# Performance work log

Measured on AMD Instinct MI355X. Metric: run time of the kernel, lower is better.

The kernel has to match this reference:

```python
import jax, jax.numpy as jnp
import numpy as np

E = 256
H_HEADS = 8
HD = E // H_HEADS
NEG = -1e9


def setup_inputs() -> dict:
    key = jax.random.key(0)
    ks = jax.random.split(key, 16)
    B, Q, Hh, Ww = 16, 100, 64, 64
    S = Hh * Ww
    std = 1.0 / np.sqrt(E)
    inp = {
        "query_features": jax.random.normal(ks[0], (B, Q, E), jnp.float32),
        "image_features": jax.random.normal(ks[1], (B, E, Hh, Ww), jnp.float32),
        "mask": jax.random.randint(ks[2], (B, Q, Hh, Ww), 0, 2) > 0,
        "pos_query_embeddings": jax.random.normal(ks[3], (B, Q, E), jnp.float32),
        "pos_image_embeddings": jax.random.normal(ks[4], (B, S, E), jnp.float32),
        "Wq": jax.random.normal(ks[5], (E, E), jnp.float32) * std,
        "bq": jnp.zeros((E,), jnp.float32),
        "Wk": jax.random.normal(ks[6], (E, E), jnp.float32) * std,
        "bk": jnp.zeros((E,), jnp.float32),
        "Wv": jax.random.normal(ks[7], (E, E), jnp.float32) * std,
        "bv": jnp.zeros((E,), jnp.float32),
        "Wo": jax.random.normal(ks[8], (E, E), jnp.float32) * std,
        "bo": jnp.zeros((E,), jnp.float32),
    }
    return inp


def reference(query_features, image_features, mask, pos_query_embeddings,
              pos_image_embeddings, Wq, bq, Wk, bk, Wv, bv, Wo, bo):
    B, _, Hh, Ww = image_features.shape
    Q = query_features.shape[1]
    S = Hh * Ww
    # (B, S, E)
    img = jnp.transpose(image_features.reshape(B, E, S), (0, 2, 1))
    q = (query_features + pos_query_embeddings) @ Wq.T + bq  # (B,Q,E)
    k = (img + pos_image_embeddings) @ Wk.T + bk              # (B,S,E)
    v = img @ Wv.T + bv                                       # (B,S,E)
    q = q.reshape(B, Q, H_HEADS, HD).transpose(0, 2, 1, 3)    # (B,H,Q,D)
    k = k.reshape(B, S, H_HEADS, HD).transpose(0, 2, 1, 3)    # (B,H,S,D)
    v = v.reshape(B, S, H_HEADS, HD).transpose(0, 2, 1, 3)
    scale = 1.0 / jnp.sqrt(jnp.asarray(HD, q.dtype))
    scores = jnp.einsum('bhqd,bhsd->bhqs', q, k) * scale
    amask = mask.reshape(B, 1, Q, S)
    scores = jnp.where(amask, scores, NEG)
    attn = jax.nn.softmax(scores, axis=-1)
    out = jnp.einsum('bhqs,bhsd->bhqd', attn, v)
    out = out.transpose(0, 2, 1, 3).reshape(B, Q, E)
    return out @ Wo.T + bo
```

## Files before the change

kernel.cpp:

```cpp
#include <hip/hip_runtime.h>
#include <math.h>

#define BB 16
#define QQ 100
#define EE 256
#define NH 8
#define HD 32
#define SS 4096
#define QP 128
#define NZ 8
#define SCHUNK (SS / NZ)
#define M0 8.0f

typedef _Float16 half8_t __attribute__((ext_vector_type(8)));
typedef _Float16 half4_t __attribute__((ext_vector_type(4)));
typedef float floatx4 __attribute__((ext_vector_type(4)));

__global__ __launch_bounds__(256) void prep_kernel(
    const float* __restrict__ qf,  const float* __restrict__ pq,
    const float* __restrict__ Wq,  const float* __restrict__ bq,
    _Float16* __restrict__ q16,
    const float* __restrict__ Wk,  const float* __restrict__ Wv,
    _Float16* __restrict__ wk16a,  _Float16* __restrict__ wv16a,
    const int* __restrict__ mask,  unsigned* __restrict__ mbits)
{
    const int bid = blockIdx.x;
    const int t = threadIdx.x;

    if (bid < 200) {
        const float scale = 0.17677669529663687f;
        const int row0 = bid * 8;
        __shared__ float xs[8][256];
        #pragma unroll
        for (int p = 0; p < 8; ++p) {
            int idx = t + p * 256;
            int f = idx & 255, j = idx >> 8;
            size_t g = (size_t)(row0 + j) * EE + f;
            xs[j][f] = qf[g] + pq[g];
        }
        __syncthreads();
        const int e = t;
        const float* wrow = Wq + (size_t)e * EE;
        float acc[8];
        const float bv = bq[e];
        #pragma unroll
        for (int j = 0; j < 8; ++j) acc[j] = bv;
        #pragma unroll 4
        for (int f4 = 0; f4 < 64; ++f4) {
            float4 w4 = *(const float4*)(wrow + f4 * 4);
            #pragma unroll
            for (int j = 0; j < 8; ++j) {
                float4 x4 = *(const float4*)&xs[j][f4 * 4];
                acc[j] = fmaf(w4.x, x4.x, acc[j]);
                acc[j] = fmaf(w4.y, x4.y, acc[j]);
                acc[j] = fmaf(w4.z, x4.z, acc[j]);
                acc[j] = fmaf(w4.w, x4.w, acc[j]);
            }
        }
        #pragma unroll
        for (int j = 0; j < 8; ++j)
            q16[(size_t)(row0 + j) * EE + e] = (_Float16)(acc[j] * scale);
    } else if (bid < 264) {
        int gid = (bid - 200) * 256 + t;
        int m = gid & 8191;
        const float* src = (gid < 8192) ? Wk : Wv;
        _Float16* dst = (gid < 8192) ? wk16a : wv16a;
        int li = m & 15, gg = (m >> 4) & 3, jj = (m >> 6) & 1;
        int kk = (m >> 7) & 7, w = (m >> 10) & 7;
        int e = w * 32 + jj * 16 + li;
        int f0 = kk * 32 + gg * 8;
        float4 a0 = *(const float4*)&src[(size_t)e * EE + f0];
        float4 a1 = *(const float4*)&src[(size_t)e * EE + f0 + 4];
        half8_t h;
        h[0]=(_Float16)a0.x; h[1]=(_Float16)a0.y; h[2]=(_Float16)a0.z; h[3]=(_Float16)a0.w;
        h[4]=(_Float16)a1.x; h[5]=(_Float16)a1.y; h[6]=(_Float16)a1.z; h[7]=(_Float16)a1.w;
        *(half8_t*)&dst[(size_t)m * 8] = h;
    } else {
        int gid  = (bid - 264) * 256 + t;
        int lane = gid & 63;
        int F    = gid & ~63;
        int s    = (F & (SS - 1)) + lane;
        int qp   = (F >> 12) & (QP - 1);
        int b    = F >> 19;
        int qc   = min(qp, QQ - 1);
        int v    = mask[((size_t)(b * QQ + qc)) * SS + s];
        unsigned long long bal = __ballot(v != 0);
        int w = (F & (SS - 1)) >> 5;
        if (lane == 0)
            mbits[((size_t)(b * (SS / 32) + w)) * QP + qp] = (unsigned)bal;
        if (lane == 32)
            mbits[((size_t)(b * (SS / 32) + w + 1)) * QP + qp] = (unsigned)(bal >> 32);
    }
}

#define KV_STEP(KK, PC, PN, AKC, AVC)                                        \
  {                                                                          \
    float pv0 = PC[l * 33 + w4 + 0];                                         \
    float pv1 = PC[l * 33 + w4 + 1];                                         \
    float pv2 = PC[l * 33 + w4 + 2];                                         \
    float pv3 = PC[l * 33 + w4 + 3];                                         \
    half4_t hk, hv;                                                          \
    hv[0] = (_Float16)iv0; hk[0] = (_Float16)(iv0 + pv0);                    \
    hv[1] = (_Float16)iv1; hk[1] = (_Float16)(iv1 + pv1);                    \
    hv[2] = (_Float16)iv2; hk[2] = (_Float16)(iv2 + pv2);                    \
    hv[3] = (_Float16)iv3; hk[3] = (_Float16)(iv3 + pv3);                    \
    *(half4_t*)&AVC[l * 40 + w4] = hv;                                       \
    *(half4_t*)&AKC[l * 40 + w4] = hk;                                       \
    if ((KK) < 7) {                                                          \
      PN[pr * 33 + pc4 + 0] = pg.x;                                          \
      PN[pr * 33 + pc4 + 1] = pg.y;                                          \
      PN[pr * 33 + pc4 + 2] = pg.z;                                          \
      PN[pr * 33 + pc4 + 3] = pg.w;                                          \
    }                                                                        \
    __syncthreads();                                                         \
    if ((KK) < 6) pg = *(const float4*)(posb + ((KK) + 2) * 32);             \
    if ((KK) < 7) {                                                          \
      iv0 = imgb[(size_t)(((KK) + 1) * 32 + w4 + 0) * SS];                   \
      iv1 = imgb[(size_t)(((KK) + 1) * 32 + w4 + 1) * SS];                   \
      iv2 = imgb[(size_t)(((KK) + 1) * 32 + w4 + 2) * SS];                   \
      iv3 = imgb[(size_t)(((KK) + 1) * 32 + w4 + 3) * SS];                   \
    }                                                                        \
    half8_t wk0 = *(const half8_t*)(wkb + (KK) * 1024);                      \
    half8_t wk1 = *(const half8_t*)(wkb + (KK) * 1024 + 512);                \
    half8_t wv0 = *(const half8_t*)(wvb + (KK) * 1024);                      \
    half8_t wv1 = *(const half8_t*)(wvb + (KK) * 1024 + 512);                \
    half8_t afk0 = *(const half8_t*)&AKC[(0 * 16 + li) * 40 + gg * 8];       \
    half8_t afk1 = *(const half8_t*)&AKC[(1 * 16 + li) * 40 + gg * 8];       \
    half8_t afk2 = *(const half8_t*)&AKC[(2 * 16 + li) * 40 + gg * 8];       \
    half8_t afk3 = *(const half8_t*)&AKC[(3 * 16 + li) * 40 + gg * 8];       \
    acck[0][0] = __builtin_amdgcn_mfma_f32_16x16x32_f16(afk0, wk0, acck[0][0], 0, 0, 0); \
    acck[0][1] = __builtin_amdgcn_mfma_f32_16x16x32_f16(afk0, wk1, acck[0][1], 0, 0, 0); \
    acck[1][0] = __builtin_amdgcn_mfma_f32_16x16x32_f16(afk1, wk0, acck[1][0], 0, 0, 0); \
    acck[1][1] = __builtin_amdgcn_mfma_f32_16x16x32_f16(afk1, wk1, acck[1][1], 0, 0, 0); \
    acck[2][0] = __builtin_amdgcn_mfma_f32_16x16x32_f16(afk2, wk0, acck[2][0], 0, 0, 0); \
    acck[2][1] = __builtin_amdgcn_mfma_f32_16x16x32_f16(afk2, wk1, acck[2][1], 0, 0, 0); \
    acck[3][0] = __builtin_amdgcn_mfma_f32_16x16x32_f16(afk3, wk0, acck[3][0], 0, 0, 0); \
    acck[3][1] = __builtin_amdgcn_mfma_f32_16x16x32_f16(afk3, wk1, acck[3][1], 0, 0, 0); \
    half8_t afv0 = *(const half8_t*)&AVC[(0 * 16 + li) * 40 + gg * 8];       \
    half8_t afv1 = *(const half8_t*)&AVC[(1 * 16 + li) * 40 + gg * 8];       \
    half8_t afv2 = *(const half8_t*)&AVC[(2 * 16 + li) * 40 + gg * 8];       \
    half8_t afv3 = *(const half8_t*)&AVC[(3 * 16 + li) * 40 + gg * 8];       \
    accv[0][0] = __builtin_amdgcn_mfma_f32_16x16x32_f16(afv0, wv0, accv[0][0], 0, 0, 0); \
    accv[0][1] = __builtin_amdgcn_mfma_f32_16x16x32_f16(afv0, wv1, accv[0][1], 0, 0, 0); \
    accv[1][0] = __builtin_amdgcn_mfma_f32_16x16x32_f16(afv1, wv0, accv[1][0], 0, 0, 0); \
    accv[1][1] = __builtin_amdgcn_mfma_f32_16x16x32_f16(afv1, wv1, accv[1][1], 0, 0, 0); \
    accv[2][0] = __builtin_amdgcn_mfma_f32_16x16x32_f16(afv2, wv0, accv[2][0], 0, 0, 0); \
    accv[2][1] = __builtin_amdgcn_mfma_f32_16x16x32_f16(afv2, wv1, accv[2][1], 0, 0, 0); \
    accv[3][0] = __builtin_amdgcn_mfma_f32_16x16x32_f16(afv3, wv0, accv[3][0], 0, 0, 0); \
    accv[3][1] = __builtin_amdgcn_mfma_f32_16x16x32_f16(afv3, wv1, accv[3][1], 0, 0, 0); \
  }

__global__ __launch_bounds__(512, 2) void fused_kv_kernel(
    const float* __restrict__ img,
    const float* __restrict__ pos,
    const _Float16* __restrict__ wk16a, const float* __restrict__ bk,
    const _Float16* __restrict__ wv16a, const float* __restrict__ bv,
    _Float16* __restrict__ kht,
    _Float16* __restrict__ vt)
{
    __shared__ __align__(16) char smem_raw[37376];
    float* posT0 = (float*)smem_raw;
    float* posT1 = posT0 + 64 * 33;
    _Float16* A0k = (_Float16*)(posT1 + 64 * 33);
    _Float16* A0v = A0k + 2560;
    _Float16* A1k = A0v + 2560;
    _Float16* A1v = A1k + 2560;

    const int t  = threadIdx.x;
    const int w  = t >> 6, l = t & 63;
    const int gg = l >> 4, li = l & 15;
    const int pr = t >> 3, pc = t & 7;
    const int w4 = w * 4, pc4 = pc * 4;

    const int m0 = blockIdx.x * 64;
    const int b  = m0 >> 12;
    const int s0 = m0 & (SS - 1);

    const float* imgb = img + (size_t)b * EE * SS + s0 + l;
    const float* posb = pos + ((size_t)(b * SS + s0 + pr)) * EE + pc4;
    const _Float16* wkb = wk16a + ((size_t)(w * 16) * 64 + l) * 8;
    const _Float16* wvb = wv16a + ((size_t)(w * 16) * 64 + l) * 8;

    floatx4 acck[4][2] = {};
    floatx4 accv[4][2] = {};

    float4 pg = *(const float4*)posb;
    float iv0 = imgb[(size_t)(w4 + 0) * SS];
    float iv1 = imgb[(size_t)(w4 + 1) * SS];
    float iv2 = imgb[(size_t)(w4 + 2) * SS];
    float iv3 = imgb[(size_t)(w4 + 3) * SS];
    posT0[pr * 33 + pc4 + 0] = pg.x;
    posT0[pr * 33 + pc4 + 1] = pg.y;
    posT0[pr * 33 + pc4 + 2] = pg.z;
    posT0[pr * 33 + pc4 + 3] = pg.w;
    pg = *(const float4*)(posb + 32);
    __syncthreads();

    #pragma unroll 1
    for (int kp = 0; kp < 4; ++kp) {
        const int kk = kp * 2;
        KV_STEP(kk,     posT0, posT1, A0k, A0v)
        KV_STEP(kk + 1, posT1, posT0, A1k, A1v)
    }

    {
        const size_t khbase = ((size_t)(b * NH + w) * SS + s0) * HD;
        #pragma unroll
        for (int jj = 0; jj < 2; ++jj) {
            int e = w * 32 + jj * 16 + li;
            int d = jj * 16 + li;
            float bj = bk[e];
            #pragma unroll
            for (int i = 0; i < 4; ++i) {
                int s_loc = i * 16 + gg * 4;
                #pragma unroll
                for (int r = 0; r < 4; ++r)
                    kht[khbase + (size_t)(s_loc + r) * HD + d] =
                        (_Float16)(acck[i][jj][r] + bj);
            }
        }
    }

    __syncthreads();
    _Float16* vstage = (_Float16*)smem_raw;
    #pragma unroll
    for (int jj = 0; jj < 2; ++jj) {
        int e_loc = w * 32 + jj * 16 + li;
        float bj = bv[e_loc];
        #pragma unroll
        for (int i = 0; i < 4; ++i) {
            int s_loc = i * 16 + gg * 4;
            half4_t h4;
            #pragma unroll
            for (int r = 0; r < 4; ++r)
                h4[r] = (_Float16)(accv[i][jj][r] + bj);
            *(half4_t*)&vstage[e_loc * 72 + s_loc] = h4;
        }
    }
    __syncthreads();
    #pragma unroll
    for (int c = 0; c < 4; ++c) {
        int row = c * 64 + (t >> 3);
        int so  = (t & 7) * 8;
        half8_t v8 = *(const half8_t*)&vstage[row * 72 + so];
        int hh = row >> 5, dd = row & 31;
        *(half8_t*)(vt + ((((size_t)(b * NH + hh) * (SS / 64) + (s0 >> 6)) * HD + dd) << 6)
                    + so) = v8;
    }
}

__global__ __launch_bounds__(256) void attn_mfma_kernel(
    const _Float16* __restrict__ q16,
    const _Float16* __restrict__ kht,
    const _Float16* __restrict__ vt,
    const unsigned* __restrict__ mbits,
    float* __restrict__ part,
    float* __restrict__ pl)
{
    const int z = blockIdx.x, h = blockIdx.y, b = blockIdx.z;
    const int t = threadIdx.x;
    const int w = t >> 6, l = t & 63;
    const int g = l >> 4, li = l & 15;

    __shared__ _Float16 ks[64 * 40];
    __shared__ _Float16 vs[32 * 72];
    __shared__ _Float16 ps[128 * 72];
    __shared__ unsigned mw[2][QP];

    half8_t qf[2];
    {
        int q0r = min(32 * w + li, QQ - 1);
        int q1r = min(32 * w + 16 + li, QQ - 1);
        qf[0] = *(const half8_t*)(q16 + ((size_t)(b * QQ + q0r)) * EE + h * HD + g * 8);
        qf[1] = *(const half8_t*)(q16 + ((size_t)(b * QQ + q1r)) * EE + h * HD + g * 8);
    }

    float lsum[2][4] = {{0.f}};
    floatx4 accO[2][2] = {};

    for (int it = 0; it < SCHUNK / 64; ++it) {
        const int sblk = z * SCHUNK + it * 64;

        {
            int sl = t >> 2, koff = (t & 3) * 8;
            *(half8_t*)&ks[sl * 40 + koff] =
                *(const half8_t*)(kht + ((size_t)(b * NH + h) * SS + sblk + sl) * HD + koff);
            int dl = t >> 3, soff = (t & 7) * 8;
            *(half8_t*)&vs[dl * 72 + soff] =
                *(const half8_t*)(vt + ((((size_t)(b * NH + h) * (SS / 64) + (sblk >> 6))
                                         * HD + dl) << 6) + soff);
            mw[t >> 7][t & 127] =
                mbits[((size_t)(b * (SS / 32) + (sblk >> 5) + (t >> 7))) * QP + (t & 127)];
        }
        __syncthreads();

        half8_t kf[4];
        #pragma unroll
        for (int st = 0; st < 4; ++st)
            kf[st] = *(const half8_t*)&ks[(st * 16 + li) * 40 + g * 8];
        floatx4 sc[2][4];
        #pragma unroll
        for (int qt = 0; qt < 2; ++qt)
            #pragma unroll
            for (int st = 0; st < 4; ++st) {
                floatx4 zero = {0.f, 0.f, 0.f, 0.f};
                sc[qt][st] = __builtin_amdgcn_mfma_f32_16x16x32_f16(
                    qf[qt], kf[st], zero, 0, 0, 0);
            }

        #pragma unroll
        for (int qt = 0; qt < 2; ++qt) {
            int qrow0 = 32 * w + qt * 16 + 4 * g;
            unsigned w0r[4], w1r[4];
            #pragma unroll
            for (int r = 0; r < 4; ++r) {
                w0r[r] = mw[0][qrow0 + r];
                w1r[r] = mw[1][qrow0 + r];
            }
            #pragma unroll
            for (int st = 0; st < 4; ++st)
                #pragma unroll
                for (int r = 0; r < 4; ++r) {
                    unsigned word = (st < 2) ? w0r[r] : w1r[r];
                    int keep = (word >> ((st & 1) * 16 + li)) & 1;
                    float pv = keep ? __expf(sc[qt][st][r] - M0) : 0.f;
                    _Float16 ph = (_Float16)pv;
                    lsum[qt][r] += (float)ph;
                    ps[(qrow0 + r) * 72 + st * 16 + li] = ph;
                }
        }

        half8_t vb[2][2];
        #pragma unroll
        for (int dt = 0; dt < 2; ++dt) {
            vb[dt][0] = *(const half8_t*)&vs[(dt * 16 + li) * 72 + g * 8];
            vb[dt][1] = *(const half8_t*)&vs[(dt * 16 + li) * 72 + 32 + g * 8];
        }
        #pragma unroll
        for (int qt = 0; qt < 2; ++qt) {
            half8_t a0 = *(const half8_t*)&ps[(32 * w + qt * 16 + li) * 72 + g * 8];
            half8_t a1 = *(const half8_t*)&ps[(32 * w + qt * 16 + li) * 72 + 32 + g * 8];
            #pragma unroll
            for (int dt = 0; dt < 2; ++dt) {
                accO[qt][dt] = __builtin_amdgcn_mfma_f32_16x16x32_f16(
                    a0, vb[dt][0], accO[qt][dt], 0, 0, 0);
                accO[qt][dt] = __builtin_amdgcn_mfma_f32_16x16x32_f16(
                    a1, vb[dt][1], accO[qt][dt], 0, 0, 0);
            }
        }
        __syncthreads();
    }

    #pragma unroll
    for (int qt = 0; qt < 2; ++qt)
        #pragma unroll
        for (int r = 0; r < 4; ++r) {
            float v = lsum[qt][r];
            v += __shfl_xor(v, 1, 64);
            v += __shfl_xor(v, 2, 64);
            v += __shfl_xor(v, 4, 64);
            v += __shfl_xor(v, 8, 64);
            lsum[qt][r] = v;
        }

    const size_t pbase = (((size_t)z * BB + b) * NH + h) * QP;
    #pragma unroll
    for (int qt = 0; qt < 2; ++qt) {
        int qrow0 = 32 * w + qt * 16 + 4 * g;
        #pragma unroll
        for (int r = 0; r < 4; ++r) {
            int qp = qrow0 + r;
            #pragma unroll
            for (int dt = 0; dt < 2; ++dt)
                part[(pbase + qp) * HD + dt * 16 + li] = accO[qt][dt][r];
            if (li == 0) pl[pbase + qp] = lsum[qt][r];
        }
    }
}

__global__ __launch_bounds__(256) void combineproj_kernel(
    const float* __restrict__ part, const float* __restrict__ pl,
    const float* __restrict__ Wo,   const float* __restrict__ bo,
    float* __restrict__ out)
{
    const int row0 = blockIdx.x * 8;
    const int t = threadIdx.x;
    __shared__ float xs[8][256];

    const int h = t >> 5, d = t & 31;
    #pragma unroll
    for (int j = 0; j < 8; ++j) {
        int row = row0 + j;
        int b = row / QQ, qp = row % QQ;
        float L = 0.f, O = 0.f;
        #pragma unroll
        for (int z = 0; z < NZ; ++z) {
            size_t idx = (((size_t)z * BB + b) * NH + h) * QP + qp;
            L += pl[idx];
            O += part[idx * HD + d];
        }
        xs[j][t] = O / fmaxf(L, 1e-30f);
    }
    __syncthreads();

    const int e = t;
    const float* wrow = Wo + (size_t)e * EE;
    float acc[8];
    const float bv = bo[e];
    #pragma unroll
    for (int j = 0; j < 8; ++j) acc[j] = bv;

    #pragma unroll 4
    for (int f4 = 0; f4 < 64; ++f4) {
        float4 w4 = *(const float4*)(wrow + f4 * 4);
        #pragma unroll
        for (int j = 0; j < 8; ++j) {
            float4 x4 = *(const float4*)&xs[j][f4 * 4];
            acc[j] = fmaf(w4.x, x4.x, acc[j]);
            acc[j] = fmaf(w4.y, x4.y, acc[j]);
            acc[j] = fmaf(w4.z, x4.z, acc[j]);
            acc[j] = fmaf(w4.w, x4.w, acc[j]);
        }
    }
    #pragma unroll
    for (int j = 0; j < 8; ++j)
        out[(size_t)(row0 + j) * EE + e] = acc[j];
}

extern "C" void kernel_launch(void* const* d_in, const int* in_sizes, int n_in,
                              void* d_out, int out_size, void* d_ws, size_t ws_size,
                              hipStream_t stream)
{
    const float* qf   = (const float*)d_in[0];
    const float* img  = (const float*)d_in[1];
    const int*   mask = (const int*)  d_in[2];
    const float* pq   = (const float*)d_in[3];
    const float* pimg = (const float*)d_in[4];
    const float* Wq   = (const float*)d_in[5];
    const float* bq   = (const float*)d_in[6];
    const float* Wk   = (const float*)d_in[7];
    const float* bk   = (const float*)d_in[8];
    const float* Wv   = (const float*)d_in[9];
    const float* bv   = (const float*)d_in[10];
    const float* Wo   = (const float*)d_in[11];
    const float* bo   = (const float*)d_in[12];
    float* out = (float*)d_out;

    const size_t MSE = (size_t)BB * SS * EE;

    _Float16* kht  = (_Float16*)d_ws;
    _Float16* vtb  = kht + MSE;
    _Float16* q16  = vtb + MSE;
    unsigned* mbits = (unsigned*)(q16 + (size_t)BB * QQ * EE);
    float* part = (float*)(mbits + (size_t)BB * (SS / 32) * QP);
    float* pl   = part + (size_t)NZ * BB * NH * QP * HD;
    _Float16* wk16a = (_Float16*)(pl + (size_t)NZ * BB * NH * QP);
    _Float16* wv16a = wk16a + (size_t)EE * EE;

    prep_kernel<<<264 + (BB * QP * SS) / 256, 256, 0, stream>>>(
        qf, pq, Wq, bq, q16, Wk, Wv, wk16a, wv16a, mask, mbits);
    fused_kv_kernel<<<BB * SS / 64, 512, 0, stream>>>(
        img, pimg, wk16a, bk, wv16a, bv, kht, vtb);
    attn_mfma_kernel<<<dim3(NZ, NH, BB), 256, 0, stream>>>(
        q16, kht, vtb, mbits, part, pl);
    combineproj_kernel<<<BB * QQ / 8, 256, 0, stream>>>(part, pl, Wo, bo, out);
}
```

Measured before the change: 281.4 us.

## Split attention by query tiles with per-wave private S streams, drop split-S partials

Restructures the attention kernel so each block handles a 32-query tile for one (b,h), with two wave pairs each walking alternate 64-key blocks over the full sequence. Each wave loads its own K/V slice into private LDS, so the per-iteration block barriers are gone. Mask words are read straight from global memory instead of being staged in LDS. The two S-halves are reduced in shared memory and the normalized output is written directly, so the combine kernel only loads rows before the output projection. This removes the NZ-way split-S partial buffers and their reduction, at the cost of reloading K/V for each of the 4 query tiles and having less per-wave reuse.

```diff
diff --git a/kernel.cpp b/kernel.cpp
--- a/kernel.cpp
+++ b/kernel.cpp
@@ -8,8 +8,6 @@
 #define HD 32
 #define SS 4096
 #define QP 128
-#define NZ 8
-#define SCHUNK (SS / NZ)
 #define M0 8.0f
 
 typedef _Float16 half8_t __attribute__((ext_vector_type(8)));
@@ -249,157 +247,148 @@
     }
 }
 
-__global__ __launch_bounds__(256) void attn_mfma_kernel(
+__global__ __launch_bounds__(256) void attn_kernel(
     const _Float16* __restrict__ q16,
     const _Float16* __restrict__ kht,
     const _Float16* __restrict__ vt,
     const unsigned* __restrict__ mbits,
-    float* __restrict__ part,
-    float* __restrict__ pl)
+    float* __restrict__ abuf)
 {
-    const int z = blockIdx.x, h = blockIdx.y, b = blockIdx.z;
+    const int qq = blockIdx.x, h = blockIdx.y, b = blockIdx.z;
     const int t = threadIdx.x;
     const int w = t >> 6, l = t & 63;
     const int g = l >> 4, li = l & 15;
-
-    __shared__ _Float16 ks[64 * 40];
-    __shared__ _Float16 vs[32 * 72];
-    __shared__ _Float16 ps[128 * 72];
-    __shared__ unsigned mw[2][QP];
-
-    half8_t qf[2];
+    const int wq = w >> 1, ws = w & 1;
+
+    __shared__ _Float16 smem[4 * 6016];
+    _Float16* Ks = smem + w * 6016;
+    _Float16* Vs = Ks + 2560;
+    _Float16* Ps = Vs + 2304;
+
+    const int qrowbase = qq * 32 + wq * 16;
+
+    half8_t qf;
     {
-        int q0r = min(32 * w + li, QQ - 1);
-        int q1r = min(32 * w + 16 + li, QQ - 1);
-        qf[0] = *(const half8_t*)(q16 + ((size_t)(b * QQ + q0r)) * EE + h * HD + g * 8);
-        qf[1] = *(const half8_t*)(q16 + ((size_t)(b * QQ + q1r)) * EE + h * HD + g * 8);
-    }
-
-    float lsum[2][4] = {{0.f}};
-    floatx4 accO[2][2] = {};
-
-    for (int it = 0; it < SCHUNK / 64; ++it) {
-        const int sblk = z * SCHUNK + it * 64;
-
+        int qr = min(qrowbase + li, QQ - 1);
+        qf = *(const half8_t*)(q16 + ((size_t)(b * QQ + qr)) * EE + h * HD + g * 8);
+    }
+
+    const _Float16* kbase = kht + (size_t)(b * NH + h) * SS * HD;
+    const _Float16* vbase = vt + (size_t)(b * NH + h) * (SS / 64) * (HD * 64);
+    const unsigned* mbase = mbits + (size_t)b * (SS / 32) * QP + qrowbase + 4 * g;
+
+    float lsum[4] = {0.f, 0.f, 0.f, 0.f};
+    floatx4 accO[2] = {};
+
+    #pragma unroll 1
+    for (int it = ws; it < 64; it += 2) {
+        const int sblk = it * 64;
         {
-            int sl = t >> 2, koff = (t & 3) * 8;
-            *(half8_t*)&ks[sl * 40 + koff] =
-                *(const half8_t*)(kht + ((size_t)(b * NH + h) * SS + sblk + sl) * HD + koff);
-            int dl = t >> 3, soff = (t & 7) * 8;
-            *(half8_t*)&vs[dl * 72 + soff] =
-                *(const half8_t*)(vt + ((((size_t)(b * NH + h) * (SS / 64) + (sblk >> 6))
-                                         * HD + dl) << 6) + soff);
-            mw[t >> 7][t & 127] =
-                mbits[((size_t)(b * (SS / 32) + (sblk >> 5) + (t >> 7))) * QP + (t & 127)];
-        }
-        __syncthreads();
-
-        half8_t kf[4];
+            const _Float16* src = kbase + (size_t)sblk * HD + l * HD;
+            #pragma unroll
+            for (int q4 = 0; q4 < 4; ++q4)
+                *(half8_t*)&Ks[l * 40 + q4 * 8] = *(const half8_t*)(src + q4 * 8);
+        }
+        {
+            int dl = l >> 1, so = (l & 1) * 32;
+            const _Float16* src = vbase + (size_t)it * (HD * 64) + dl * 64 + so;
+            #pragma unroll
+            for (int q4 = 0; q4 < 4; ++q4)
+                *(half8_t*)&Vs[dl * 72 + so + q4 * 8] = *(const half8_t*)(src + q4 * 8);
+        }
+        uint4 mw0 = *(const uint4*)(mbase + (size_t)(it * 2) * QP);
+        uint4 mw1 = *(const uint4*)(mbase + (size_t)(it * 2 + 1) * QP);
+
+        half8_t kf0 = *(const half8_t*)&Ks[(0 * 16 + li) * 40 + g * 8];
+        half8_t kf1 = *(const half8_t*)&Ks[(1 * 16 + li) * 40 + g * 8];
+        half8_t kf2 = *(const half8_t*)&Ks[(2 * 16 + li) * 40 + g * 8];
+        half8_t kf3 = *(const half8_t*)&Ks[(3 * 16 + li) * 40 + g * 8];
+        floatx4 zero = {0.f, 0.f, 0.f, 0.f};
+        floatx4 sc[4];
+        sc[0] = __builtin_amdgcn_mfma_f32_16x16x32_f16(qf, kf0, zero, 0, 0, 0);
+        sc[1] = __builtin_amdgcn_mfma_f32_16x16x32_f16(qf, kf1, zero, 0, 0, 0);
+        sc[2] = __builtin_amdgcn_mfma_f32_16x16x32_f16(qf, kf2, zero, 0, 0, 0);
+        sc[3] = __builtin_amdgcn_mfma_f32_16x16x32_f16(qf, kf3, zero, 0, 0, 0);
+
+        unsigned mr0[4] = {mw0.x, mw0.y, mw0.z, mw0.w};
+        unsigned mr1[4] = {mw1.x, mw1.y, mw1.z, mw1.w};
         #pragma unroll
         for (int st = 0; st < 4; ++st)
-            kf[st] = *(const half8_t*)&ks[(st * 16 + li) * 40 + g * 8];
-        floatx4 sc[2][4];
-        #pragma unroll
-        for (int qt = 0; qt < 2; ++qt)
-            #pragma unroll
-            for (int st = 0; st < 4; ++st) {
-                floatx4 zero = {0.f, 0.f, 0.f, 0.f};
-                sc[qt][st] = __builtin_amdgcn_mfma_f32_16x16x32_f16(
-                    qf[qt], kf[st], zero, 0, 0, 0);
+            #pragma unroll
+            for (int r = 0; r < 4; ++r) {
+                unsigned word = (st < 2) ? mr0[r] : mr1[r];
+                int keep = (word >> ((st & 1) * 16 + li)) & 1;
+                float pv = keep ? __expf(sc[st][r] - M0) : 0.f;
+                _Float16 ph = (_Float16)pv;
+                lsum[r] += (float)ph;
+                Ps[(4 * g + r) * 72 + st * 16 + li] = ph;
             }
 
-        #pragma unroll
-        for (int qt = 0; qt < 2; ++qt) {
-            int qrow0 = 32 * w + qt * 16 + 4 * g;
-            unsigned w0r[4], w1r[4];
-            #pragma unroll
-            for (int r = 0; r < 4; ++r) {
-                w0r[r] = mw[0][qrow0 + r];
-                w1r[r] = mw[1][qrow0 + r];
+        half8_t a0 = *(const half8_t*)&Ps[li * 72 + g * 8];
+        half8_t a1 = *(const half8_t*)&Ps[li * 72 + 32 + g * 8];
+        #pragma unroll
+        for (int dt = 0; dt < 2; ++dt) {
+            half8_t vb0 = *(const half8_t*)&Vs[(dt * 16 + li) * 72 + g * 8];
+            half8_t vb1 = *(const half8_t*)&Vs[(dt * 16 + li) * 72 + 32 + g * 8];
+            accO[dt] = __builtin_amdgcn_mfma_f32_16x16x32_f16(a0, vb0, accO[dt], 0, 0, 0);
+            accO[dt] = __builtin_amdgcn_mfma_f32_16x16x32_f16(a1, vb1, accO[dt], 0, 0, 0);
+        }
+    }
+
+    #pragma unroll
+    for (int r = 0; r < 4; ++r) {
+        float v = lsum[r];
+        v += __shfl_xor(v, 1, 64);
+        v += __shfl_xor(v, 2, 64);
+        v += __shfl_xor(v, 4, 64);
+        v += __shfl_xor(v, 8, 64);
+        lsum[r] = v;
+    }
+
+    __syncthreads();
+    float* redO = (float*)smem;
+    float* redl = redO + 2 * 16 * 32;
+    if (ws == 1) {
+        #pragma unroll
+        for (int r = 0; r < 4; ++r) {
+            int q = 4 * g + r;
+            redO[(wq * 16 + q) * 32 + li]      = accO[0][r];
+            redO[(wq * 16 + q) * 32 + 16 + li] = accO[1][r];
+            if (li == 0) redl[wq * 16 + q] = lsum[r];
+        }
+    }
+    __syncthreads();
+    if (ws == 0) {
+        #pragma unroll
+        for (int r = 0; r < 4; ++r) {
+            int q = 4 * g + r;
+            int qglob = qrowbase + q;
+            float L = lsum[r] + redl[wq * 16 + q];
+            float invL = 1.f / fmaxf(L, 1e-30f);
+            if (qglob < QQ) {
+                float o0 = (accO[0][r] + redO[(wq * 16 + q) * 32 + li]) * invL;
+                float o1 = (accO[1][r] + redO[(wq * 16 + q) * 32 + 16 + li]) * invL;
+                abuf[((size_t)(b * QQ + qglob)) * EE + h * HD + li]      = o0;
+                abuf[((size_t)(b * QQ + qglob)) * EE + h * HD + 16 + li] = o1;
             }
-            #pragma unroll
-            for (int st = 0; st < 4; ++st)
-                #pragma unroll
-                for (int r = 0; r < 4; ++r) {
-                    unsigned word = (st < 2) ? w0r[r] : w1r[r];
-                    int keep = (word >> ((st & 1) * 16 + li)) & 1;
-                    float pv = keep ? __expf(sc[qt][st][r] - M0) : 0.f;
-                    _Float16 ph = (_Float16)pv;
-                    lsum[qt][r] += (float)ph;
-                    ps[(qrow0 + r) * 72 + st * 16 + li] = ph;
-                }
-        }
-
-        half8_t vb[2][2];
-        #pragma unroll
-        for (int dt = 0; dt < 2; ++dt) {
-            vb[dt][0] = *(const half8_t*)&vs[(dt * 16 + li) * 72 + g * 8];
-            vb[dt][1] = *(const half8_t*)&vs[(dt * 16 + li) * 72 + 32 + g * 8];
-        }
-        #pragma unroll
-        for (int qt = 0; qt < 2; ++qt) {
-            half8_t a0 = *(const half8_t*)&ps[(32 * w + qt * 16 + li) * 72 + g * 8];
-            half8_t a1 = *(const half8_t*)&ps[(32 * w + qt * 16 + li) * 72 + 32 + g * 8];
-            #pragma unroll
-            for (int dt = 0; dt < 2; ++dt) {
-                accO[qt][dt] = __builtin_amdgcn_mfma_f32_16x16x32_f16(
-                    a0, vb[dt][0], accO[qt][dt], 0, 0, 0);
-                accO[qt][dt] = __builtin_amdgcn_mfma_f32_16x16x32_f16(
-                    a1, vb[dt][1], accO[qt][dt], 0, 0, 0);
-            }
-        }
-        __syncthreads();
-    }
-
-    #pragma unroll
-    for (int qt = 0; qt < 2; ++qt)
-        #pragma unroll
-        for (int r = 0; r < 4; ++r) {
-            float v = lsum[qt][r];
-            v += __shfl_xor(v, 1, 64);
-            v += __shfl_xor(v, 2, 64);
-            v += __shfl_xor(v, 4, 64);
-            v += __shfl_xor(v, 8, 64);
-            lsum[qt][r] = v;
-        }
-
-    const size_t pbase = (((size_t)z * BB + b) * NH + h) * QP;
-    #pragma unroll
-    for (int qt = 0; qt < 2; ++qt) {
-        int qrow0 = 32 * w + qt * 16 + 4 * g;
-        #pragma unroll
-        for (int r = 0; r < 4; ++r) {
-            int qp = qrow0 + r;
-            #pragma unroll
-            for (int dt = 0; dt < 2; ++dt)
-                part[(pbase + qp) * HD + dt * 16 + li] = accO[qt][dt][r];
-            if (li == 0) pl[pbase + qp] = lsum[qt][r];
         }
     }
 }
 
-__global__ __launch_bounds__(256) void combineproj_kernel(
-    const float* __restrict__ part, const float* __restrict__ pl,
-    const float* __restrict__ Wo,   const float* __restrict__ bo,
+__global__ __launch_bounds__(256) void projo_kernel(
+    const float* __restrict__ abuf,
+    const float* __restrict__ Wo, const float* __restrict__ bo,
     float* __restrict__ out)
 {
     const int row0 = blockIdx.x * 8;
     const int t = threadIdx.x;
     __shared__ float xs[8][256];
 
-    const int h = t >> 5, d = t & 31;
-    #pragma unroll
-    for (int j = 0; j < 8; ++j) {
-        int row = row0 + j;
-        int b = row / QQ, qp = row % QQ;
-        float L = 0.f, O = 0.f;
-        #pragma unroll
-        for (int z = 0; z < NZ; ++z) {
-            size_t idx = (((size_t)z * BB + b) * NH + h) * QP + qp;
-            L += pl[idx];
-            O += part[idx * HD + d];
-        }
-        xs[j][t] = O / fmaxf(L, 1e-30f);
+    #pragma unroll
+    for (int p = 0; p < 8; ++p) {
+        int idx = t + p * 256;
+        int f = idx & 255, j = idx >> 8;
+        xs[j][f] = abuf[(size_t)(row0 + j) * EE + f];
     }
     __syncthreads();
 
@@ -452,16 +441,15 @@
     _Float16* vtb  = kht + MSE;
     _Float16* q16  = vtb + MSE;
     unsigned* mbits = (unsigned*)(q16 + (size_t)BB * QQ * EE);
-    float* part = (float*)(mbits + (size_t)BB * (SS / 32) * QP);
-    float* pl   = part + (size_t)NZ * BB * NH * QP * HD;
-    _Float16* wk16a = (_Float16*)(pl + (size_t)NZ * BB * NH * QP);
+    float* abuf = (float*)(mbits + (size_t)BB * (SS / 32) * QP);
+    _Float16* wk16a = (_Float16*)(abuf + (size_t)BB * QQ * EE);
     _Float16* wv16a = wk16a + (size_t)EE * EE;
 
     prep_kernel<<<264 + (BB * QP * SS) / 256, 256, 0, stream>>>(
         qf, pq, Wq, bq, q16, Wk, Wv, wk16a, wv16a, mask, mbits);
     fused_kv_kernel<<<BB * SS / 64, 512, 0, stream>>>(
         img, pimg, wk16a, bk, wv16a, bv, kht, vtb);
-    attn_mfma_kernel<<<dim3(NZ, NH, BB), 256, 0, stream>>>(
-        q16, kht, vtb, mbits, part, pl);
-    combineproj_kernel<<<BB * QQ / 8, 256, 0, stream>>>(part, pl, Wo, bo, out);
+    attn_kernel<<<dim3(4, NH, BB), 256, 0, stream>>>(
+        q16, kht, vtb, mbits, abuf);
+    projo_kernel<<<BB * QQ / 8, 256, 0, stream>>>(abuf, Wo, bo, out);
 }
```

After: 287.9 us. 2.3% more time.
